# Performance work log

Hardware: AMD Instinct MI355X
Metric: run time of the kernel (lower is better)

The kernel has to match this reference:

```python
import jax, jax.numpy as jnp
import numpy as np

D_MODEL = 1024
NUM_HEADS = 16
D_K = D_MODEL // NUM_HEADS
THETA = 10000.0
BATCH, SEQ = 2, 2048


def setup_inputs() -> dict:
    key = jax.random.key(0)
    k1, k2, k3 = jax.random.split(key, 3)
    x = jax.random.normal(k1, (BATCH, SEQ, D_MODEL), dtype=jnp.float32)
    token_positions = jnp.arange(SEQ, dtype=jnp.int64 if jax.config.jax_enable_x64 else jnp.int32)
    # torch.nn.Linear convention: weight [out_features, in_features], y = x @ W.T
    w_qkv = jax.random.normal(k2, (3 * D_MODEL, D_MODEL), dtype=jnp.float32) * 0.02
    w_o = jax.random.normal(k3, (D_MODEL, D_MODEL), dtype=jnp.float32) * 0.02
    return {"x": x, "token_positions": token_positions, "w_qkv": w_qkv, "w_o": w_o}


def _rope(v, positions):
    # v: [B, H, S, d_k]; positions: [S] int
    half = D_K // 2
    inv_freq = THETA ** (-jnp.arange(0, half, dtype=jnp.float32) / half)  # [half]
    angles = positions.astype(jnp.float32)[:, None] * inv_freq[None, :]   # [S, half]
    cos = jnp.cos(angles)  # [S, half]
    sin = jnp.sin(angles)
    v1 = v[..., 0::2]  # even dims [B,H,S,half]
    v2 = v[..., 1::2]  # odd dims
    r1 = v1 * cos - v2 * sin
    r2 = v1 * sin + v2 * cos
    # interleave back to [..., d_k]
    return jnp.stack([r1, r2], axis=-1).reshape(v.shape)


def reference(x, token_positions, w_qkv, w_o):
    B, S, _ = x.shape
    # fused QKV projection: [B,S,3*D] -> [B,S,3,H,d_k]
    qkv = jnp.einsum("bsd,ed->bse", x, w_qkv).reshape(B, S, 3, NUM_HEADS, D_K)
    q = jnp.transpose(qkv[:, :, 0], (0, 2, 1, 3))
    k = jnp.transpose(qkv[:, :, 1], (0, 2, 1, 3))
    v = jnp.transpose(qkv[:, :, 2], (0, 2, 1, 3))
    q = _rope(q, token_positions)
    k = _rope(k, token_positions)
    scale = 1.0 / jnp.sqrt(jnp.float32(D_K))
    scores = jnp.einsum("bhqd,bhkd->bhqk", q, k) * scale  # [B,H,S,S]
    causal = jnp.tril(jnp.ones((S, S), dtype=bool))
    scores = jnp.where(causal, scores, jnp.float32(-jnp.inf))
    attn = jax.nn.softmax(scores, axis=-1)
    out = jnp.einsum("bhqk,bhkd->bhqd", attn, v)  # [B,H,S,d_k]
    out = jnp.transpose(out, (0, 2, 1, 3)).reshape(B, S, D_MODEL)
    return jnp.einsum("bsd,ed->bse", out, w_o)
```

## Files before the change

### kernel.cpp

```cpp
#include <hip/hip_runtime.h>
#include <cstdint>
#include <cstddef>

#define D_MODEL 1024
#define NHEADS  16
#define DK      64
#define SEQ     2048
#define NBATCH  2

#define NEG_BIG (-1e30f)

typedef __attribute__((ext_vector_type(8))) short bf16x8;
typedef __attribute__((ext_vector_type(4))) short bf16x4;
typedef __attribute__((ext_vector_type(4))) float f32x4;

#if defined(__AMDGCN__)
#define SETPRIO(p) __builtin_amdgcn_s_setprio(p)
#else
#define SETPRIO(p)
#endif

__device__ inline f32x4 mfma16x16x16(bf16x4 a, bf16x4 b, f32x4 c) {
#if defined(__AMDGCN__)
# if __has_builtin(__builtin_amdgcn_mfma_f32_16x16x16_bf16)
  return __builtin_amdgcn_mfma_f32_16x16x16_bf16(a, b, c, 0, 0, 0);
# else
  return __builtin_amdgcn_mfma_f32_16x16x16bf16_1k(a, b, c, 0, 0, 0);
# endif
#else
  (void)a; (void)b;
  return c;
#endif
}

__device__ inline void gll16(const unsigned short* g, unsigned short* l) {
#if defined(__AMDGCN__)
  __builtin_amdgcn_global_load_lds(
      (const __attribute__((address_space(1))) void*)g,
      (__attribute__((address_space(3))) void*)l, 16, 0, 0);
#else
  (void)g; (void)l;
#endif
}

__device__ inline unsigned short f2bf(float f) {
  unsigned int u = __float_as_uint(f);
  u += 0x7fffu + ((u >> 16) & 1u);
  return (unsigned short)(u >> 16);
}

__device__ __forceinline__ void cvt_block(const void* src,
                                          unsigned short* dst, int i0) {
  const unsigned short* sp =
      (const unsigned short*)src + (size_t)i0 * 8 + threadIdx.x * 8;
  int cnt = 0;
#pragma unroll
  for (int j = 0; j < 8; j += 2) {
    const unsigned int u = sp[j];
    cnt += (((u >> 7) & 0xFFu) >= 0x84u) ? 1 : 0;
  }
  __shared__ int red[256];
  red[threadIdx.x] = cnt;
  __syncthreads();
  for (int s = 128; s > 0; s >>= 1) {
    if (threadIdx.x < s) red[threadIdx.x] += red[threadIdx.x + s];
    __syncthreads();
  }
  const bool isf32 = red[0] > 64;

  const int i = i0 + threadIdx.x;
  if (isf32) {
    const float4* s = (const float4*)src;
    float4 a = s[2 * i], b = s[2 * i + 1];
    uint4 r;
    r.x = (unsigned)f2bf(a.x) | ((unsigned)f2bf(a.y) << 16);
    r.y = (unsigned)f2bf(a.z) | ((unsigned)f2bf(a.w) << 16);
    r.z = (unsigned)f2bf(b.x) | ((unsigned)f2bf(b.y) << 16);
    r.w = (unsigned)f2bf(b.z) | ((unsigned)f2bf(b.w) << 16);
    ((uint4*)dst)[i] = r;
  } else {
    ((uint4*)dst)[i] = ((const uint4*)src)[i];
  }
}

__global__ __launch_bounds__(256) void cvt2_kernel(
    const void* __restrict__ srcA, unsigned short* __restrict__ dstA, int n8A,
    const void* __restrict__ srcB, unsigned short* __restrict__ dstB, int n8B) {
  const int bi = blockIdx.x;
  const int nblkA = n8A >> 8;
  (void)n8B;
  if (bi < nblkA) cvt_block(srcA, dstA, bi << 8);
  else            cvt_block(srcB, dstB, (bi - nblkA) << 8);
}

__global__ __launch_bounds__(256) void cvt3_kernel(
    const void* __restrict__ srcA, unsigned short* __restrict__ dstA, int n8A,
    const void* __restrict__ srcB, unsigned short* __restrict__ dstB, int n8B,
    const void* __restrict__ srcC, unsigned short* __restrict__ dstC) {
  const int bi = blockIdx.x;
  const int nblkA = n8A >> 8;
  const int nblkB = n8B >> 8;
  if (bi < nblkA)               cvt_block(srcA, dstA, bi << 8);
  else if (bi < nblkA + nblkB)  cvt_block(srcB, dstB, (bi - nblkA) << 8);
  else                          cvt_block(srcC, dstC, (bi - nblkA - nblkB) << 8);
}

template <int NF>
__device__ inline void gemm_bt_t(const unsigned short* __restrict__ A,
                                 const unsigned short* __restrict__ W,
                                 int m0, int n0,
                                 unsigned short* As, unsigned short* Bs,
                                 f32x4 (&acc)[NF][4]) {
  const int t    = threadIdx.x;
  const int lane = t & 63;
  const int w    = t >> 6;
  const int wm   = (w >> 1) * 64;
  const int wn   = (w & 1) * (NF * 16);
  const int frow = lane & 15;
  const int q4   = lane >> 4;

  for (int ft = 0; ft < NF; ++ft)
    for (int tt = 0; tt < 4; ++tt)
      acc[ft][tt] = (f32x4){0.f, 0.f, 0.f, 0.f};

  const int srow  = t >> 3;
  const int gslot = t & 7;

  for (int k0 = 0; k0 < 1024; k0 += 64) {
    __syncthreads();
#pragma unroll
    for (int c = 0; c < 4; ++c) {
      const int row = c * 32 + srow;
      const int gsrc = gslot ^ (row & 7);
      gll16(A + (size_t)(m0 + row) * 1024 + k0 + gsrc * 8,
            As + ((size_t)t + 256 * c) * 8);
    }
#pragma unroll
    for (int c = 0; c < NF; ++c) {
      const int row = c * 32 + srow;
      const int gsrc = gslot ^ (row & 7);
      gll16(W + (size_t)(n0 + row) * 1024 + k0 + gsrc * 8,
            Bs + ((size_t)t + 256 * c) * 8);
    }
    __syncthreads();

#pragma unroll
    for (int kk = 0; kk < 2; ++kk) {
      const int gg = q4 + kk * 4;
      bf16x8 xv[4], wv[NF];
#pragma unroll
      for (int tt = 0; tt < 4; ++tt) {
        const int row = wm + tt * 16 + frow;
        xv[tt] = *(const bf16x8*)(As + row * 64 + ((gg ^ (row & 7)) << 3));
      }
#pragma unroll
      for (int ft = 0; ft < NF; ++ft) {
        const int row = wn + ft * 16 + frow;
        wv[ft] = *(const bf16x8*)(Bs + row * 64 + ((gg ^ (row & 7)) << 3));
      }
#pragma unroll
      for (int ft = 0; ft < NF; ++ft)
#pragma unroll
        for (int tt = 0; tt < 4; ++tt)
          acc[ft][tt] = __builtin_amdgcn_mfma_f32_16x16x32_bf16(wv[ft], xv[tt],
                                                                acc[ft][tt], 0, 0, 0);
    }
  }
}

__global__ __launch_bounds__(256) void qkv_rope_kernel(
    const unsigned short* __restrict__ x,
    const unsigned short* __restrict__ wqkv,
    unsigned short* __restrict__ Qw, unsigned short* __restrict__ Kw,
    unsigned short* __restrict__ Vw) {
  __shared__ __align__(16) unsigned short As[128 * 64];
  __shared__ __align__(16) unsigned short Bs[128 * 64];
  f32x4 acc[4][4];
  const int lin = blockIdx.y * 32 + blockIdx.x;
  const int c8  = lin & 7;
  const int i   = lin >> 3;
  const int m0  = (c8 * 4 + (i & 3)) * 128;
  const int n0  = (i >> 2) * 128;
  gemm_bt_t<4>(x, wqkv, m0, n0, As, Bs, acc);

  const int t = threadIdx.x, lane = t & 63, w = t >> 6;
  const int wm = (w >> 1) * 64, wn = (w & 1) * 64;
  const int i16 = lane & 15, q4 = lane >> 4;
  const int part = n0 >> 10;
  unsigned short* dst = (part == 0) ? Qw : ((part == 1) ? Kw : Vw);
  const float LN_THETA_OVER_HALF = 0.2878231366242558f;

#pragma unroll
  for (int ft = 0; ft < 4; ++ft) {
    const int nb0 = n0 + wn + ft * 16 + (q4 << 2);
    const int h  = (nb0 >> 6) & 15;
    const int d0 = nb0 & 63;
    const float invf0 = __expf(-(float)(d0 >> 1) * LN_THETA_OVER_HALF);
    const float invf1 = __expf(-(float)((d0 >> 1) + 1) * LN_THETA_OVER_HALF);
#pragma unroll
    for (int tt = 0; tt < 4; ++tt) {
      const int m = m0 + wm + tt * 16 + i16;
      const int b = m >> 11, s = m & 2047;
      float v0 = acc[ft][tt][0], v1 = acc[ft][tt][1];
      float v2 = acc[ft][tt][2], v3 = acc[ft][tt][3];
      if (part < 2) {
        float sn0, cs0, sn1, cs1;
        __sincosf((float)s * invf0, &sn0, &cs0);
        __sincosf((float)s * invf1, &sn1, &cs1);
        const float r0 = v0 * cs0 - v1 * sn0;
        const float r1 = v0 * sn0 + v1 * cs0;
        const float r2 = v2 * cs1 - v3 * sn1;
        const float r3 = v2 * sn1 + v3 * cs1;
        v0 = r0; v1 = r1; v2 = r2; v3 = r3;
        if (part == 0) { v0 *= 0.125f; v1 *= 0.125f; v2 *= 0.125f; v3 *= 0.125f; }
      }
      ushort4 pk;
      pk.x = f2bf(v0); pk.y = f2bf(v1); pk.z = f2bf(v2); pk.w = f2bf(v3);
      *(ushort4*)(dst + (((size_t)(b * NHEADS + h)) * SEQ + s) * DK + d0) = pk;
    }
  }
}

__device__ __forceinline__ void attn_step(
    const unsigned short* Ks0, const unsigned short* Ks1,
    const unsigned short* Vt0, const unsigned short* Vt1,
    bf16x8 qf0, bf16x8 qf1, int i16, int q4, int w,
    int q0t, int kt2, bool domask,
    float& m_i, float& l_i, f32x4 o_acc[4]) {
  f32x4 s_acc[2][4];
  SETPRIO(1);
#pragma unroll
  for (int u = 0; u < 2; ++u) {
    const unsigned short* Ksu = u ? Ks1 : Ks0;
#pragma unroll
    for (int mt = 0; mt < 4; ++mt) {
      const int key = mt * 16 + i16;
      const int k7 = key & 7;
      bf16x8 a0 = *(const bf16x8*)(Ksu + key * 64 + ((q4 ^ k7) << 3));
      bf16x8 a1 = *(const bf16x8*)(Ksu + key * 64 + (((4 + q4) ^ k7) << 3));
      f32x4 acc = (f32x4){0.f, 0.f, 0.f, 0.f};
      acc = __builtin_amdgcn_mfma_f32_16x16x32_bf16(a0, qf0, acc, 0, 0, 0);
      acc = __builtin_amdgcn_mfma_f32_16x16x32_bf16(a1, qf1, acc, 0, 0, 0);
      s_acc[u][mt] = acc;
    }
  }
  SETPRIO(0);

  if (domask) {
    const int qrow = q0t + w * 16 + i16;
#pragma unroll
    for (int u = 0; u < 2; ++u) {
      const int kb2 = (kt2 + u) * 64 + q4 * 4;
#pragma unroll
      for (int mt = 0; mt < 4; ++mt)
#pragma unroll
        for (int r = 0; r < 4; ++r)
          if (kb2 + mt * 16 + r > qrow) s_acc[u][mt][r] = NEG_BIG;
    }
  }

  float tm = NEG_BIG;
#pragma unroll
  for (int u = 0; u < 2; ++u)
#pragma unroll
    for (int mt = 0; mt < 4; ++mt)
#pragma unroll
      for (int r = 0; r < 4; ++r) tm = fmaxf(tm, s_acc[u][mt][r]);
  tm = fmaxf(tm, __shfl_xor(tm, 16, 64));
  tm = fmaxf(tm, __shfl_xor(tm, 32, 64));
  const float m_new = fmaxf(m_i, tm);
  const float alpha = __expf(m_i - m_new);
  m_i = m_new;

  bf16x4 pf[2][4];
  float ls = 0.f;
#pragma unroll
  for (int u = 0; u < 2; ++u)
#pragma unroll
    for (int mt = 0; mt < 4; ++mt) {
      float p0 = __expf(s_acc[u][mt][0] - m_new);
      float p1 = __expf(s_acc[u][mt][1] - m_new);
      float p2 = __expf(s_acc[u][mt][2] - m_new);
      float p3 = __expf(s_acc[u][mt][3] - m_new);
      ls += (p0 + p1) + (p2 + p3);
      pf[u][mt][0] = (short)f2bf(p0);
      pf[u][mt][1] = (short)f2bf(p1);
      pf[u][mt][2] = (short)f2bf(p2);
      pf[u][mt][3] = (short)f2bf(p3);
    }
  ls += __shfl_xor(ls, 16, 64);
  ls += __shfl_xor(ls, 32, 64);
  l_i = l_i * alpha + ls;

  float a4[4];
#pragma unroll
  for (int r = 0; r < 4; ++r) a4[r] = __shfl(alpha, (q4 << 2) + r, 64);
#pragma unroll
  for (int n = 0; n < 4; ++n)
#pragma unroll
    for (int r = 0; r < 4; ++r) o_acc[n][r] *= a4[r];

  SETPRIO(1);
#pragma unroll
  for (int u = 0; u < 2; ++u) {
    const unsigned short* Vtu = u ? Vt1 : Vt0;
#pragma unroll
    for (int mt = 0; mt < 4; ++mt) {
#pragma unroll
      for (int nt = 0; nt < 4; ++nt) {
        const int dk = nt * 16 + i16;
        const int slot = ((mt << 1) | (q4 >> 1)) ^ (dk & 7);
        bf16x4 vb = *(const bf16x4*)(Vtu + dk * 64 + (slot << 3) + ((q4 & 1) << 2));
        o_acc[nt] = mfma16x16x16(pf[u][mt], vb, o_acc[nt]);
      }
    }
  }
  SETPRIO(0);
}

__global__ __launch_bounds__(256) void attn_mfma_kernel(
    const unsigned short* __restrict__ Q, const unsigned short* __restrict__ K,
    const unsigned short* __restrict__ V, unsigned short* __restrict__ O) {
  __shared__ __align__(16) unsigned short Ks[2][64 * 64];
  __shared__ __align__(16) unsigned short Vt[2][64 * 64];

  const int t = threadIdx.x, w = t >> 6, lane = t & 63;
  const int i16 = lane & 15, q4 = lane >> 4;
  const int bh = blockIdx.y;
  const int qbA = blockIdx.x;
  const int qbB = 31 - blockIdx.x;
  const int q0A = qbA * 64, q0B = qbB * 64;
  const size_t base = (size_t)bh * SEQ * DK;

  bf16x8 qfA0, qfA1, qfB0, qfB1;
  {
    const unsigned short* qpA = Q + base + (size_t)(q0A + w * 16 + i16) * DK + q4 * 8;
    qfA0 = *(const bf16x8*)(qpA);
    qfA1 = *(const bf16x8*)(qpA + 32);
    const unsigned short* qpB = Q + base + (size_t)(q0B + w * 16 + i16) * DK + q4 * 8;
    qfB0 = *(const bf16x8*)(qpB);
    qfB1 = *(const bf16x8*)(qpB + 32);
  }

  f32x4 oA[4], oB[4];
#pragma unroll
  for (int n = 0; n < 4; ++n) {
    oA[n] = (f32x4){0.f, 0.f, 0.f, 0.f};
    oB[n] = (f32x4){0.f, 0.f, 0.f, 0.f};
  }
  float mA = NEG_BIG, lA = 0.f, mB = NEG_BIG, lB = 0.f;

  const int krow = t >> 2;
  const int kc   = (t & 3) << 1;
  const int kr7  = krow & 7;
  const int vu   = t >> 7;
  const int tl   = t & 127;
  const int vkq  = (tl & 15) << 2;
  const int vd8  = (tl >> 4) << 3;
  const int vg   = vkq >> 3;
  const int vh   = (vkq >> 2) & 1;

  const int npairA = (qbA >> 1) + 1;
  const int npairB = (qbB >> 1) + 1;

  for (int pr = 0; pr < npairB; ++pr) {
    const int kt2 = pr * 2;
    __syncthreads();
#pragma unroll
    for (int u = 0; u < 2; ++u) {
      const unsigned short* kp =
          K + base + (size_t)((kt2 + u) * 64 + krow) * DK + (kc << 3);
      uint4 k0 = *(const uint4*)kp;
      uint4 k1 = *(const uint4*)(kp + 8);
      *(uint4*)(Ks[u] + krow * 64 + ((kc ^ kr7) << 3))       = k0;
      *(uint4*)(Ks[u] + krow * 64 + (((kc + 1) ^ kr7) << 3)) = k1;
    }
    {
      const unsigned short* vp =
          V + base + (size_t)((kt2 + vu) * 64 + vkq) * DK + vd8;
      uint4 u0 = *(const uint4*)(vp);
      uint4 u1 = *(const uint4*)(vp + DK);
      uint4 u2 = *(const uint4*)(vp + 2 * DK);
      uint4 u3 = *(const uint4*)(vp + 3 * DK);
      const unsigned short* a0 = (const unsigned short*)&u0;
      const unsigned short* a1 = (const unsigned short*)&u1;
      const unsigned short* a2 = (const unsigned short*)&u2;
      const unsigned short* a3 = (const unsigned short*)&u3;
#pragma unroll
      for (int j = 0; j < 8; ++j) {
        const int dk = vd8 + j;
        const int slot = vg ^ (dk & 7);
        ushort4 pk;
        pk.x = a0[j]; pk.y = a1[j]; pk.z = a2[j]; pk.w = a3[j];
        *(ushort4*)(Vt[vu] + dk * 64 + (slot << 3) + (vh << 2)) = pk;
      }
    }
    __syncthreads();

    attn_step(Ks[0], Ks[1], Vt[0], Vt[1], qfB0, qfB1, i16, q4, w,
              q0B, kt2, pr == npairB - 1, mB, lB, oB);
    if (pr < npairA)
      attn_step(Ks[0], Ks[1], Vt[0], Vt[1], qfA0, qfA1, i16, q4, w,
                q0A, kt2, pr == npairA - 1, mA, lA, oA);
  }

  const int b = bh >> 4, h = bh & 15;
#pragma unroll
  for (int r = 0; r < 4; ++r) {
    const float lrA = __shfl(lA, (q4 << 2) + r, 64);
    const float lrB = __shfl(lB, (q4 << 2) + r, 64);
    const float invA = 1.0f / lrA;
    const float invB = 1.0f / lrB;
    const int sA = q0A + w * 16 + (q4 << 2) + r;
    const int sB = q0B + w * 16 + (q4 << 2) + r;
#pragma unroll
    for (int nt = 0; nt < 4; ++nt) {
      const int dk = nt * 16 + i16;
      O[((size_t)(b * SEQ + sA)) * D_MODEL + h * DK + dk] = f2bf(oA[nt][r] * invA);
      O[((size_t)(b * SEQ + sB)) * D_MODEL + h * DK + dk] = f2bf(oB[nt][r] * invB);
    }
  }
}

__global__ __launch_bounds__(256) void oproj_kernel(
    const unsigned short* __restrict__ ain, const unsigned short* __restrict__ wo,
    float* __restrict__ out) {
  __shared__ __align__(16) unsigned short As[128 * 64];
  __shared__ __align__(16) unsigned short Bs[64 * 64];
  f32x4 acc[2][4];
  const int lin = blockIdx.y * 32 + blockIdx.x;
  const int c8  = lin & 7;
  const int i   = lin >> 3;
  const int m0  = (c8 * 4 + (i & 3)) * 128;
  const int n0  = (i >> 2) * 64;
  gemm_bt_t<2>(ain, wo, m0, n0, As, Bs, acc);

  const int t = threadIdx.x, lane = t & 63, w = t >> 6;
  const int wm = (w >> 1) * 64, wn = (w & 1) * 32;
  const int i16 = lane & 15, q4 = lane >> 4;
#pragma unroll
  for (int ft = 0; ft < 2; ++ft) {
    const int nb0 = n0 + wn + ft * 16 + (q4 << 2);
#pragma unroll
    for (int tt = 0; tt < 4; ++tt) {
      const int m = m0 + wm + tt * 16 + i16;
      float4 v;
      v.x = acc[ft][tt][0]; v.y = acc[ft][tt][1];
      v.z = acc[ft][tt][2]; v.w = acc[ft][tt][3];
      *(float4*)(out + (size_t)m * D_MODEL + nb0) = v;
    }
  }
}

extern "C" void kernel_launch(void* const* d_in, const int* in_sizes, int n_in,
                              void* d_out, int out_size, void* d_ws, size_t ws_size,
                              hipStream_t stream) {
  const void* x    = d_in[0];
  const void* wqkv = d_in[2];
  const void* wo   = d_in[3];
  float* out = (float*)d_out;

  const size_t NTOK  = (size_t)NBATCH * SEQ * D_MODEL;
  const size_t NWQKV = (size_t)3 * D_MODEL * D_MODEL;
  const size_t NWO   = (size_t)D_MODEL * D_MODEL;

  unsigned short* base = (unsigned short*)((char*)d_ws + 16);
  unsigned short* Qw = base;
  unsigned short* Kw = Qw + NTOK;
  unsigned short* Vw = Kw + NTOK;
  unsigned short* Aw = Vw + NTOK;
  unsigned short* xb = Aw;
  unsigned short* wq = Aw + NTOK;

  dim3 blk(256);

  const size_t need = 16 + (4 * NTOK + NWQKV + NWO) * sizeof(unsigned short);

  if (ws_size >= need) {
    unsigned short* wb = wq + NWQKV;
    hipLaunchKernelGGL(cvt3_kernel, dim3(4096), blk, 0, stream,
                       x, xb, (int)(NTOK / 8), wqkv, wq, (int)(NWQKV / 8),
                       wo, wb);

    dim3 g1(32, 24);
    hipLaunchKernelGGL(qkv_rope_kernel, g1, blk, 0, stream, xb, wq, Qw, Kw, Vw);

    dim3 g2(SEQ / 128, NBATCH * NHEADS);
    hipLaunchKernelGGL(attn_mfma_kernel, g2, blk, 0, stream, Qw, Kw, Vw, Aw);

    dim3 g3(32, 16);
    hipLaunchKernelGGL(oproj_kernel, g3, blk, 0, stream, Aw, wb, out);
  } else {
    unsigned short* wb = wq;
    hipLaunchKernelGGL(cvt2_kernel, dim3(3584), blk, 0, stream,
                       x, xb, (int)(NTOK / 8), wqkv, wq, (int)(NWQKV / 8));

    dim3 g1(32, 24);
    hipLaunchKernelGGL(qkv_rope_kernel, g1, blk, 0, stream, xb, wq, Qw, Kw, Vw);

    dim3 g2(SEQ / 128, NBATCH * NHEADS);
    hipLaunchKernelGGL(attn_mfma_kernel, g2, blk, 0, stream, Qw, Kw, Vw, Aw);

    hipLaunchKernelGGL(cvt2_kernel, dim3(512), blk, 0, stream,
                       wo, wb, (int)(NWO / 8), wo, wb, 0);

    dim3 g3(32, 16);
    hipLaunchKernelGGL(oproj_kernel, g3, blk, 0, stream, Aw, wb, out);
  }
}
```

Measured before the change: 207.4 us.

## Store V transposed and double-buffer K/V tiles with async global-to-LDS loads

The QKV projection epilogue now writes V in a transposed [b,h,d,s] layout. This lets the attention kernel stage K and V tiles straight into shared memory with direct global-to-LDS loads instead of transposing V through registers. The attention loop double-buffers these tiles and issues the next pair's loads before computing on the current pair, aiming to hide global latency and drop one barrier per iteration. In exchange, shared memory use doubles and V is written as scattered 2-byte stores. Correctness also relies on the async loads completing before the barrier.

```diff
diff --git a/kernel.cpp b/kernel.cpp
--- a/kernel.cpp
+++ b/kernel.cpp
@@ -187,7 +187,6 @@
   const int wm = (w >> 1) * 64, wn = (w & 1) * 64;
   const int i16 = lane & 15, q4 = lane >> 4;
   const int part = n0 >> 10;
-  unsigned short* dst = (part == 0) ? Qw : ((part == 1) ? Kw : Vw);
   const float LN_THETA_OVER_HALF = 0.2878231366242558f;
 
 #pragma unroll
@@ -213,10 +212,18 @@
         const float r3 = v2 * sn1 + v3 * cs1;
         v0 = r0; v1 = r1; v2 = r2; v3 = r3;
         if (part == 0) { v0 *= 0.125f; v1 *= 0.125f; v2 *= 0.125f; v3 *= 0.125f; }
+        ushort4 pk;
+        pk.x = f2bf(v0); pk.y = f2bf(v1); pk.z = f2bf(v2); pk.w = f2bf(v3);
+        unsigned short* dst = (part == 0) ? Qw : Kw;
+        *(ushort4*)(dst + (((size_t)(b * NHEADS + h)) * SEQ + s) * DK + d0) = pk;
+      } else {
+        unsigned short* vt =
+            Vw + (((size_t)(b * NHEADS + h)) * DK + d0) * SEQ + s;
+        vt[0]       = f2bf(v0);
+        vt[SEQ]     = f2bf(v1);
+        vt[2 * SEQ] = f2bf(v2);
+        vt[3 * SEQ] = f2bf(v3);
       }
-      ushort4 pk;
-      pk.x = f2bf(v0); pk.y = f2bf(v1); pk.z = f2bf(v2); pk.w = f2bf(v3);
-      *(ushort4*)(dst + (((size_t)(b * NHEADS + h)) * SEQ + s) * DK + d0) = pk;
     }
   }
 }
@@ -320,9 +327,9 @@
 
 __global__ __launch_bounds__(256) void attn_mfma_kernel(
     const unsigned short* __restrict__ Q, const unsigned short* __restrict__ K,
-    const unsigned short* __restrict__ V, unsigned short* __restrict__ O) {
-  __shared__ __align__(16) unsigned short Ks[2][64 * 64];
-  __shared__ __align__(16) unsigned short Vt[2][64 * 64];
+    const unsigned short* __restrict__ VT, unsigned short* __restrict__ O) {
+  __shared__ __align__(16) unsigned short Ks[2][2][64 * 64];
+  __shared__ __align__(16) unsigned short Vt[2][2][64 * 64];
 
   const int t = threadIdx.x, w = t >> 6, lane = t & 63;
   const int i16 = lane & 15, q4 = lane >> 4;
@@ -331,6 +338,27 @@
   const int qbB = 31 - blockIdx.x;
   const int q0A = qbA * 64, q0B = qbB * 64;
   const size_t base = (size_t)bh * SEQ * DK;
+
+  const int srow  = t >> 3;
+  const int gslot = t & 7;
+
+  auto stage = [&](int p, int buf) {
+#pragma unroll
+    for (int c = 0; c < 4; ++c) {
+      const int row = srow + 32 * c;
+      const int gs  = gslot ^ (row & 7);
+      gll16(K + base + (size_t)(p * 128 + row) * DK + gs * 8,
+            &Ks[buf][0][0] + ((size_t)t + 256 * c) * 8);
+    }
+#pragma unroll
+    for (int c = 0; c < 4; ++c) {
+      const int row = srow + 32 * c;
+      const int gs  = gslot ^ (row & 7);
+      gll16(VT + base + (size_t)(row & 63) * SEQ
+               + p * 128 + (row >> 6) * 64 + gs * 8,
+            &Vt[buf][0][0] + ((size_t)t + 256 * c) * 8);
+    }
+  };
 
   bf16x8 qfA0, qfA1, qfB0, qfB1;
   {
@@ -350,58 +378,22 @@
   }
   float mA = NEG_BIG, lA = 0.f, mB = NEG_BIG, lB = 0.f;
 
-  const int krow = t >> 2;
-  const int kc   = (t & 3) << 1;
-  const int kr7  = krow & 7;
-  const int vu   = t >> 7;
-  const int tl   = t & 127;
-  const int vkq  = (tl & 15) << 2;
-  const int vd8  = (tl >> 4) << 3;
-  const int vg   = vkq >> 3;
-  const int vh   = (vkq >> 2) & 1;
-
   const int npairA = (qbA >> 1) + 1;
   const int npairB = (qbB >> 1) + 1;
 
+  stage(0, 0);
+
   for (int pr = 0; pr < npairB; ++pr) {
     const int kt2 = pr * 2;
+    const int cb = pr & 1;
     __syncthreads();
-#pragma unroll
-    for (int u = 0; u < 2; ++u) {
-      const unsigned short* kp =
-          K + base + (size_t)((kt2 + u) * 64 + krow) * DK + (kc << 3);
-      uint4 k0 = *(const uint4*)kp;
-      uint4 k1 = *(const uint4*)(kp + 8);
-      *(uint4*)(Ks[u] + krow * 64 + ((kc ^ kr7) << 3))       = k0;
-      *(uint4*)(Ks[u] + krow * 64 + (((kc + 1) ^ kr7) << 3)) = k1;
-    }
-    {
-      const unsigned short* vp =
-          V + base + (size_t)((kt2 + vu) * 64 + vkq) * DK + vd8;
-      uint4 u0 = *(const uint4*)(vp);
-      uint4 u1 = *(const uint4*)(vp + DK);
-      uint4 u2 = *(const uint4*)(vp + 2 * DK);
-      uint4 u3 = *(const uint4*)(vp + 3 * DK);
-      const unsigned short* a0 = (const unsigned short*)&u0;
-      const unsigned short* a1 = (const unsigned short*)&u1;
-      const unsigned short* a2 = (const unsigned short*)&u2;
-      const unsigned short* a3 = (const unsigned short*)&u3;
-#pragma unroll
-      for (int j = 0; j < 8; ++j) {
-        const int dk = vd8 + j;
-        const int slot = vg ^ (dk & 7);
-        ushort4 pk;
-        pk.x = a0[j]; pk.y = a1[j]; pk.z = a2[j]; pk.w = a3[j];
-        *(ushort4*)(Vt[vu] + dk * 64 + (slot << 3) + (vh << 2)) = pk;
-      }
-    }
-    __syncthreads();
-
-    attn_step(Ks[0], Ks[1], Vt[0], Vt[1], qfB0, qfB1, i16, q4, w,
-              q0B, kt2, pr == npairB - 1, mB, lB, oB);
+    if (pr + 1 < npairB) stage(pr + 1, cb ^ 1);
+
+    attn_step(Ks[cb][0], Ks[cb][1], Vt[cb][0], Vt[cb][1], qfB0, qfB1,
+              i16, q4, w, q0B, kt2, pr == npairB - 1, mB, lB, oB);
     if (pr < npairA)
-      attn_step(Ks[0], Ks[1], Vt[0], Vt[1], qfA0, qfA1, i16, q4, w,
-                q0A, kt2, pr == npairA - 1, mA, lA, oA);
+      attn_step(Ks[cb][0], Ks[cb][1], Vt[cb][0], Vt[cb][1], qfA0, qfA1,
+                i16, q4, w, q0A, kt2, pr == npairA - 1, mA, lA, oA);
   }
 
   const int b = bh >> 4, h = bh & 15;
```

New measurement: 191.7 us. 7.6% less time.
